# Kernel optimization log

Measured on AMD Instinct MI355X. Metric: run time of the kernel, lower is better.

Reference implementation:

```python
import jax, jax.numpy as jnp
import numpy as np

D_MODEL = 1024
C_OUT = 64
PRED_LEN = 96
D_STATE = 64
D_CONV = 4
EXPAND = 2
D_INNER = EXPAND * D_MODEL          # 2048
DT_RANK = D_MODEL // 16             # 64
IN_DIM = D_MODEL + C_OUT
BATCH = 512


def setup_inputs() -> dict:
    key = jax.random.key(0)
    ks = jax.random.split(key, 10)
    def w(k, shape, scale=0.02):
        return jax.random.normal(k, shape, dtype=jnp.float32) * scale
    return {
        "context": jax.random.normal(ks[0], (BATCH, D_MODEL), dtype=jnp.float32),
        "initial_values": jax.random.normal(ks[1], (BATCH, C_OUT), dtype=jnp.float32),
        "w_in": w(ks[2], (IN_DIM, 2 * D_INNER)),
        "b_in": jnp.zeros((2 * D_INNER,), jnp.float32),
        "conv_w": w(ks[3], (D_INNER, D_CONV)),
        "conv_b": jnp.zeros((D_INNER,), jnp.float32),
        "w_x": w(ks[4], (D_INNER, DT_RANK + 2 * D_STATE)),
        "w_dt": w(ks[5], (DT_RANK, D_INNER)),
        "b_dt": jnp.zeros((D_INNER,), jnp.float32),
        "A_log": jnp.log(jnp.broadcast_to(jnp.arange(1, D_STATE + 1, dtype=jnp.float32), (D_INNER, D_STATE))),
        "D_skip": jnp.ones((D_INNER,), jnp.float32),
        "w_out": w(ks[6], (D_INNER, D_MODEL)),
        "b_out": jnp.zeros((D_MODEL,), jnp.float32),
        "w_proj": w(ks[7], (D_MODEL, C_OUT)),
        "b_proj": jnp.zeros((C_OUT,), jnp.float32),
    }


def _mamba_len1(u, w_in, b_in, conv_w, conv_b, w_x, w_dt, b_dt, D_skip, w_out, b_out):
    """Standard Mamba block applied to a length-1 sequence (fresh state each call,
    matching the torch module, which calls mamba on [B,1,D] every step).
    With h0 = 0 and L = 1, the exp(dt*A) recurrence term vanishes, so A_log has no effect."""
    xz = u @ w_in + b_in                         # [B, 2*D_INNER]
    x, z = jnp.split(xz, 2, axis=-1)             # [B, D_INNER] each
    # causal depthwise conv over L=1: only the last kernel tap hits the current input
    x = x * conv_w[:, -1] + conv_b
    x = jax.nn.silu(x)
    xdbc = x @ w_x                               # [B, DT_RANK + 2*D_STATE]
    dt = jax.nn.softplus(xdbc[:, :DT_RANK] @ w_dt + b_dt)          # [B, D_INNER]
    Bm = xdbc[:, DT_RANK:DT_RANK + D_STATE]                         # [B, D_STATE]
    Cm = xdbc[:, DT_RANK + D_STATE:]                                # [B, D_STATE]
    # h = (dt*x)[:, :, None] * Bm[:, None, :]; y = sum_s h * Cm  ->  factored form
    y = (dt * x) * jnp.sum(Bm * Cm, axis=-1, keepdims=True)         # [B, D_INNER]
    y = y + D_skip * x
    y = y * jax.nn.silu(z)
    return y @ w_out + b_out                     # [B, D_MODEL]


def reference(context, initial_values, w_in, b_in, conv_w, conv_b, w_x, w_dt,
              b_dt, A_log, D_skip, w_out, b_out, w_proj, b_proj):
    del A_log  # no effect with fresh zero SSM state and seq_len=1 (see _mamba_len1)

    def step(prev_pred, _):
        u = jnp.concatenate([context, prev_pred], axis=-1)          # [B, IN_DIM]
        h = _mamba_len1(u, w_in, b_in, conv_w, conv_b, w_x, w_dt, b_dt,
                        D_skip, w_out, b_out)                        # [B, D_MODEL]
        pred = h @ w_proj + b_proj                                   # [B, C_OUT]
        return pred, pred

    _, preds = jax.lax.scan(step, initial_values, None, length=PRED_LEN)
    return jnp.transpose(preds, (1, 0, 2))       # [B, PRED_LEN, C_OUT]
```

## Files before the change

kernel.cpp:

```cpp
#include <hip/hip_runtime.h>
#include <math.h>


typedef __fp16 half2_t __attribute__((ext_vector_type(2)));
typedef unsigned int uint32;
union HU { uint32 u; half2_t h; };

__device__ __forceinline__ float sigf(float v){
  return __builtin_amdgcn_rcpf(1.f + __expf(-v));
}
__device__ __forceinline__ uint32 pk2(float a, float b){
  HU x; x.h = __builtin_amdgcn_cvt_pkrtz(a, b); return x.u;
}
__device__ __forceinline__ float dot2(uint32 a, uint32 b, float c){
  HU ua, ub; ua.u = a; ub.u = b;
  return __builtin_amdgcn_fdot2(ua.h, ub.h, c, false);
}


__global__ __launch_bounds__(256) void k_ctx(
    const float* __restrict__ ctxin, const float* __restrict__ w_in,
    const float* __restrict__ b_in, float* __restrict__ ctx_xz){
  int tid = threadIdx.x;
  int j = blockIdx.x*256 + tid;
  int b0 = blockIdx.y*16;
  const float* cp = ctxin + (size_t)b0*1024;
  float acc[16];
#pragma unroll
  for (int r=0;r<16;r++) acc[r]=0.f;
  for (int k=0;k<1024;k+=4){
    float w0 = w_in[(size_t)(k+0)*4096 + j];
    float w1 = w_in[(size_t)(k+1)*4096 + j];
    float w2 = w_in[(size_t)(k+2)*4096 + j];
    float w3 = w_in[(size_t)(k+3)*4096 + j];
#pragma unroll
    for (int r=0;r<16;r++){
      acc[r] += cp[r*1024+k]*w0 + cp[r*1024+k+1]*w1
              + cp[r*1024+k+2]*w2 + cp[r*1024+k+3]*w3;
    }
  }
  float bj = b_in[j];
#pragma unroll
  for (int r=0;r<16;r++) ctx_xz[(size_t)(b0+r)*4096 + j] = acc[r] + bj;
}

__global__ __launch_bounds__(256) void k_wop(
    const float* __restrict__ w_out, const float* __restrict__ w_proj,
    const float* __restrict__ b_out, const float* __restrict__ b_proj,
    float* __restrict__ W_op, float* __restrict__ b_op){
  int g = blockIdx.x, tid = threadIdx.x;
  if (g == 512){
    if (tid < 64){
      float s = b_proj[tid];
      for (int k=0;k<1024;k++) s += b_out[k]*w_proj[k*64+tid];
      b_op[tid] = s;
    }
    return;
  }
  int idx = g*256 + tid;
  int c = idx>>6, o = idx&63;
  float s = 0.f;
  const float* wr = w_out + (size_t)c*1024;
  for (int k=0;k<1024;k++) s += wr[k]*w_proj[k*64+o];
  W_op[idx] = s;
}

__global__ __launch_bounds__(256) void k_cvec(
    const float* __restrict__ b_op, const float* __restrict__ w_in2,
    float* __restrict__ cvec){
  int j = blockIdx.x*256 + threadIdx.x;
  float s = 0.f;
  for (int o=0;o<64;o++) s += b_op[o]*w_in2[(size_t)o*4096 + j];
  cvec[j] = s;
}

__global__ __launch_bounds__(256) void k_pack(
    const float* __restrict__ src, uint32* __restrict__ dst,
    int inner, int total){
  int idx = blockIdx.x*256 + threadIdx.x;
  if (idx >= total) return;
  int p = idx / inner, i = idx - p*inner;
  dst[idx] = pk2(src[(size_t)(2*p)*inner + i], src[(size_t)(2*p+1)*inner + i]);
}

__global__ __launch_bounds__(256) void k_pack_wx(
    const float* __restrict__ w_x, uint32* __restrict__ dst){
  int idx = blockIdx.x*256 + threadIdx.x;
  int q = idx & 3;
  int t = idx >> 2;
  int n = t % 192;
  int g = t / 192;
  int k2 = g*4 + q;
  dst[idx] = pk2(w_x[(size_t)(2*k2)*192 + n], w_x[(size_t)(2*k2+1)*192 + n]);
}

__global__ __launch_bounds__(256) void k_pack_wop(
    const float* __restrict__ W_op, uint32* __restrict__ dst){
  int idx = blockIdx.x*256 + threadIdx.x;
  int q = idx & 3;
  int t = idx >> 2;
  int o = t & 63;
  int g = t >> 6;
  int k2 = g*4 + q;
  dst[idx] = pk2(W_op[(size_t)(2*k2)*64 + o], W_op[(size_t)(2*k2+1)*64 + o]);
}

__global__ __launch_bounds__(256) void k_pack_wdt(
    const float* __restrict__ w_dt, uint32* __restrict__ dst){
  int idx = blockIdx.x*256 + threadIdx.x;
  int e = idx & 3;
  int t = idx >> 2;
  int c2 = t & 1023;
  int jp = t >> 10;
  int p = jp*2 + (e>>1);
  int c = c2*2 + (e&1);
  dst[idx] = pk2(w_dt[(size_t)(2*p)*2048 + c], w_dt[(size_t)(2*p+1)*2048 + c]);
}


__global__ __launch_bounds__(1024,4) void k_steps(
    const float* __restrict__ ctx_xz, const float* __restrict__ cvec,
    const uint32* __restrict__ h_in2p, const float* __restrict__ conv_w,
    const float* __restrict__ conv_b,  const uint32* __restrict__ wxp4,
    const uint32* __restrict__ wdtp4,  const float* __restrict__ b_dt,
    const float* __restrict__ D_skip,  const uint32* __restrict__ wopp4,
    const float* __restrict__ b_op,    const float* __restrict__ initial,
    float* __restrict__ dout)
{
  const int tid = threadIdx.x;
  const int r0  = blockIdx.x * 2;

  __shared__ uint2  predH2[32];
  __shared__ __align__(16) uint32 xbufH[2][1024];
  __shared__ float  zbuf[2][2048];
  __shared__ uint4  xdh2q[16];
  __shared__ float  bcL[2];
  __shared__ float  pxd[4][388];
  __shared__ float  ppd[16][130];
  __shared__ uint4  wxpin[6144];

  {
    const uint4* src = (const uint4*)wxp4;
#pragma unroll
    for (int i = tid; i < 6144; i += 1024){
      int ks = i / 1536;
      wxpin[i] = src[i + ks*10752];
    }
  }

  const int cb = tid*4;
  const bool isx = (cb < 2048);
  float4 cw4, cb4;
  if (isx){
    cw4 = make_float4(conv_w[(cb+0)*4+3], conv_w[(cb+1)*4+3],
                      conv_w[(cb+2)*4+3], conv_w[(cb+3)*4+3]);
    cb4 = *(const float4*)&conv_b[cb];
  }
  const float4 cv4   = *(const float4*)&cvec[cb];
  const float4 ctxr0 = *(const float4*)&ctx_xz[(size_t)(r0+0)*4096 + cb];
  const float4 ctxr1 = *(const float4*)&ctx_xz[(size_t)(r0+1)*4096 + cb];
  const int c2t = tid*2;
  const float2 bdt2 = *(const float2*)&b_dt[c2t];
  const float2 dsk2 = *(const float2*)&D_skip[c2t];
  const int n2  = tid % 192;
  const int ks2 = tid / 192;
  const int o4  = tid & 63;
  const int kb2 = (tid >> 6) * 64;
  const float bopv = b_op[(tid>>1) & 63];

  if (tid < 128){
    float v = initial[(size_t)(r0 + (tid&1))*64 + (tid>>1)];
    float vp = __shfl_down(v, 2, 64);
    if ((tid & 2) == 0)
      ((uint32*)predH2)[(tid>>2)*2 + (tid&1)] = pk2(v, vp);
  }
  __syncthreads();

  for (int t=0; t<96; t++){
    const float tf = (t > 0) ? 1.f : 0.f;
    float a0[4], a1[4];
#pragma unroll
    for (int i=0;i<4;i++){
      float c = (&cv4.x)[i];
      a0[i] = (&ctxr0.x)[i] + tf*c;
      a1[i] = (&ctxr1.x)[i] + tf*c;
    }
    {
      const uint32* wp = h_in2p + cb;
#pragma unroll 8
      for (int o2=0;o2<32;o2++){
        uint4 w  = *(const uint4*)&wp[(size_t)o2*4096];
        uint2 pd = *((const uint2*)predH2 + o2);
        a0[0]=dot2(w.x,pd.x,a0[0]); a0[1]=dot2(w.y,pd.x,a0[1]);
        a0[2]=dot2(w.z,pd.x,a0[2]); a0[3]=dot2(w.w,pd.x,a0[3]);
        a1[0]=dot2(w.x,pd.y,a1[0]); a1[1]=dot2(w.y,pd.y,a1[1]);
        a1[2]=dot2(w.z,pd.y,a1[2]); a1[3]=dot2(w.w,pd.y,a1[3]);
      }
    }
    if (isx){
      float x0[4], x1[4];
#pragma unroll
      for (int i=0;i<4;i++){
        float v0 = a0[i]*(&cw4.x)[i] + (&cb4.x)[i];
        float v1 = a1[i]*(&cw4.x)[i] + (&cb4.x)[i];
        x0[i] = v0*sigf(v0);
        x1[i] = v1*sigf(v1);
      }
      const int p = cb >> 1;
      *(uint2*)&xbufH[0][p] = make_uint2(pk2(x0[0], x0[1]), pk2(x0[2], x0[3]));
      *(uint2*)&xbufH[1][p] = make_uint2(pk2(x1[0], x1[1]), pk2(x1[2], x1[3]));
    } else {
      float4 z0, z1;
#pragma unroll
      for (int i=0;i<4;i++){
        (&z0.x)[i] = a0[i]*sigf(a0[i]);
        (&z1.x)[i] = a1[i]*sigf(a1[i]);
      }
      *(float4*)&zbuf[0][cb-2048] = z0;
      *(float4*)&zbuf[1][cb-2048] = z1;
    }
    __syncthreads();

    if (tid < 768){
      const uint4* wpin = &wxpin[ks2*1536 + n2];
      const uint4* wp4  = (const uint4*)wxp4 + (size_t)ks2*12288 + n2;
      const uint4* xb0  = (const uint4*)&xbufH[0][ks2*256];
      const uint4* xb1  = (const uint4*)&xbufH[1][ks2*256];
      float f0 = 0.f, f1 = 0.f;
#pragma unroll
      for (int j=0;j<8;j++){
        uint4 w  = wpin[j*192];
        uint4 x0 = xb0[j];
        uint4 x1 = xb1[j];
        f0 = dot2(w.x, x0.x, f0); f1 = dot2(w.x, x1.x, f1);
        f0 = dot2(w.y, x0.y, f0); f1 = dot2(w.y, x1.y, f1);
        f0 = dot2(w.z, x0.z, f0); f1 = dot2(w.z, x1.z, f1);
        f0 = dot2(w.w, x0.w, f0); f1 = dot2(w.w, x1.w, f1);
      }
#pragma unroll 8
      for (int j=8;j<64;j++){
        uint4 w  = wp4[(size_t)j*192];
        uint4 x0 = xb0[j];
        uint4 x1 = xb1[j];
        f0 = dot2(w.x, x0.x, f0); f1 = dot2(w.x, x1.x, f1);
        f0 = dot2(w.y, x0.y, f0); f1 = dot2(w.y, x1.y, f1);
        f0 = dot2(w.z, x0.z, f0); f1 = dot2(w.z, x1.z, f1);
        f0 = dot2(w.w, x0.w, f0); f1 = dot2(w.w, x1.w, f1);
      }
      *(float2*)&pxd[ks2][n2*2] = make_float2(f0, f1);
    }
    __syncthreads();

    if (tid < 128){
      int r = tid >> 6, nl = tid & 63;
      int ib = (64+nl)*2 + r, ic = (128+nl)*2 + r;
      float bv = pxd[0][ib] + pxd[1][ib] + pxd[2][ib] + pxd[3][ib];
      float cv = pxd[0][ic] + pxd[1][ic] + pxd[2][ic] + pxd[3][ic];
      float p = bv * cv;
#pragma unroll
      for (int sh=1; sh<64; sh<<=1) p += __shfl_xor(p, sh, 64);
      if (nl == 0) bcL[r] = p;
    } else if (tid < 160){
      int o2 = tid - 128;
      int i00 = (2*o2)*2, i10 = (2*o2+1)*2;
      float v00 = pxd[0][i00  ] + pxd[1][i00  ] + pxd[2][i00  ] + pxd[3][i00  ];
      float v01 = pxd[0][i00+1] + pxd[1][i00+1] + pxd[2][i00+1] + pxd[3][i00+1];
      float v10 = pxd[0][i10  ] + pxd[1][i10  ] + pxd[2][i10  ] + pxd[3][i10  ];
      float v11 = pxd[0][i10+1] + pxd[1][i10+1] + pxd[2][i10+1] + pxd[3][i10+1];
      ((uint32*)xdh2q)[o2*2+0] = pk2(v00, v10);
      ((uint32*)xdh2q)[o2*2+1] = pk2(v01, v11);
    }
    __syncthreads();

    float d00=0.f, d01=0.f, d10=0.f, d11=0.f;
    {
      const uint4* wd4 = (const uint4*)wdtp4 + tid;
#pragma unroll 8
      for (int jp=0;jp<16;jp++){
        uint4 w  = wd4[(size_t)jp*1024];
        uint4 xd = xdh2q[jp];
        d00 = dot2(w.x, xd.x, d00);
        d01 = dot2(w.y, xd.x, d01);
        d10 = dot2(w.x, xd.y, d10);
        d11 = dot2(w.y, xd.y, d11);
        d00 = dot2(w.z, xd.z, d00);
        d01 = dot2(w.w, xd.z, d01);
        d10 = dot2(w.z, xd.w, d10);
        d11 = dot2(w.w, xd.w, d11);
      }
    }
    {
      float bc0 = bcL[0], bc1 = bcL[1];
      HU xh0, xh1; xh0.u = xbufH[0][tid]; xh1.u = xbufH[1][tid];
      float2 zr0 = *(const float2*)&zbuf[0][c2t];
      float2 zr1 = *(const float2*)&zbuf[1][c2t];
      float v00 = d00 + bdt2.x, v01 = d01 + bdt2.y;
      float v10 = d10 + bdt2.x, v11 = d11 + bdt2.y;
      float s00 = (v00 > 15.f) ? v00 : __logf(1.f + __expf(v00));
      float s01 = (v01 > 15.f) ? v01 : __logf(1.f + __expf(v01));
      float s10 = (v10 > 15.f) ? v10 : __logf(1.f + __expf(v10));
      float s11 = (v11 > 15.f) ? v11 : __logf(1.f + __expf(v11));
      float y00 = (s00*bc0 + dsk2.x) * (float)xh0.h.x * zr0.x;
      float y01 = (s01*bc0 + dsk2.y) * (float)xh0.h.y * zr0.y;
      float y10 = (s10*bc1 + dsk2.x) * (float)xh1.h.x * zr1.x;
      float y11 = (s11*bc1 + dsk2.y) * (float)xh1.h.y * zr1.y;
      xbufH[0][tid] = pk2(y00, y01);
      xbufH[1][tid] = pk2(y10, y11);
    }
    __syncthreads();

    {
      const uint4* wo4 = (const uint4*)wopp4 + (size_t)(tid>>6)*1024 + o4;
      const uint4* yb0 = (const uint4*)&xbufH[0][kb2];
      const uint4* yb1 = (const uint4*)&xbufH[1][kb2];
      float p0 = 0.f, p1 = 0.f;
#pragma unroll 8
      for (int j=0;j<16;j++){
        uint4 w  = wo4[(size_t)j*64];
        uint4 y0 = yb0[j];
        uint4 y1 = yb1[j];
        p0 = dot2(w.x, y0.x, p0); p1 = dot2(w.x, y1.x, p1);
        p0 = dot2(w.y, y0.y, p0); p1 = dot2(w.y, y1.y, p1);
        p0 = dot2(w.z, y0.z, p0); p1 = dot2(w.z, y1.z, p1);
        p0 = dot2(w.w, y0.w, p0); p1 = dot2(w.w, y1.w, p1);
      }
      *(float2*)&ppd[tid>>6][o4*2] = make_float2(p0, p1);
    }
    __syncthreads();

    if (tid < 128){
      float v = 0.f;
#pragma unroll
      for (int ks=0; ks<16; ks++) v += ppd[ks][tid];
      int o = tid >> 1, r = tid & 1;
      dout[((size_t)(r0+r)*96 + t)*64 + o] = v + bopv;
      float vp = __shfl_down(v, 2, 64);
      if ((tid & 2) == 0)
        ((uint32*)predH2)[(tid>>2)*2 + (tid&1)] = pk2(v, vp);
    }
    __syncthreads();
  }
}


extern "C" void kernel_launch(void* const* d_in, const int* in_sizes, int n_in,
                              void* d_out, int out_size, void* d_ws, size_t ws_size,
                              hipStream_t stream)
{
  const float* context = (const float*)d_in[0];
  const float* initial = (const float*)d_in[1];
  const float* w_in    = (const float*)d_in[2];
  const float* b_in    = (const float*)d_in[3];
  const float* conv_w  = (const float*)d_in[4];
  const float* conv_b  = (const float*)d_in[5];
  const float* w_x     = (const float*)d_in[6];
  const float* w_dt    = (const float*)d_in[7];
  const float* b_dt    = (const float*)d_in[8];
  const float* D_skip  = (const float*)d_in[10];
  const float* w_out   = (const float*)d_in[11];
  const float* b_out   = (const float*)d_in[12];
  const float* w_proj  = (const float*)d_in[13];
  const float* b_proj  = (const float*)d_in[14];

  float* ws = (float*)d_ws;
  float*  ctx_xz = ws;
  float*  cvec   = ctx_xz + 2097152;
  float*  W_op   = cvec + 4096;
  float*  b_op   = W_op + 131072;
  uint32* h_in2p = (uint32*)(b_op + 128);
  uint32* wxp4   = h_in2p + 131072;
  uint32* wdtp4  = wxp4 + 196608;
  uint32* wopp4  = wdtp4 + 65536;
  float*  dout   = (float*)d_out;

  const float* w_in2 = w_in + (size_t)1024*4096;

  k_wop     <<<dim3(513),   256, 0, stream>>>(w_out, w_proj, b_out, b_proj, W_op, b_op);
  k_cvec    <<<dim3(16),    256, 0, stream>>>(b_op, w_in2, cvec);
  k_ctx     <<<dim3(16,32), 256, 0, stream>>>(context, w_in, b_in, ctx_xz);
  k_pack    <<<dim3(512),   256, 0, stream>>>(w_in2, h_in2p, 4096, 131072);
  k_pack_wx <<<dim3(768),   256, 0, stream>>>(w_x,  wxp4);
  k_pack_wdt<<<dim3(256),   256, 0, stream>>>(w_dt, wdtp4);
  k_pack_wop<<<dim3(256),   256, 0, stream>>>(W_op, wopp4);

  k_steps<<<dim3(256), 1024, 0, stream>>>(ctx_xz, cvec, h_in2p, conv_w, conv_b,
                                          wxp4, wdtp4, b_dt, D_skip, wopp4, b_op,
                                          initial, dout);
}
```

Before: 2.082 ms.

## Replace per-step block barriers with redundant per-wave reductions and private LDS buffers

Two of the `__syncthreads` calls per time step are removed. Every wavefront now redundantly computes the B·C dot product, the packed dt-rank vector and the next prediction vector into its own LDS slot (`xdh2qW`, `predH2W`), so no cross-wave hand-off is needed. An `s_waitcnt lgkmcnt(0)` fence orders the LDS accesses within each wave, and the output store becomes a float2 store from wave 0. This trades extra redundant LDS reads and ALU work across 16 waves for fewer block-wide barriers in the 96-step serial loop.

```diff
diff --git a/kernel.cpp b/kernel.cpp
--- a/kernel.cpp
+++ b/kernel.cpp
@@ -15,6 +15,9 @@
 __device__ __forceinline__ float dot2(uint32 a, uint32 b, float c){
   HU ua, ub; ua.u = a; ub.u = b;
   return __builtin_amdgcn_fdot2(ua.h, ub.h, c, false);
+}
+__device__ __forceinline__ void ldsfence(){
+  asm volatile("s_waitcnt lgkmcnt(0)" ::: "memory");
 }
 
 
@@ -127,21 +130,21 @@
     const float* __restrict__ b_op,    const float* __restrict__ initial,
     float* __restrict__ dout)
 {
-  const int tid = threadIdx.x;
-  const int r0  = blockIdx.x * 2;
-
-  __shared__ uint2  predH2[32];
+  const int tid  = threadIdx.x;
+  const int wid  = tid >> 6;
+  const int lane = tid & 63;
+  const int r0   = blockIdx.x * 2;
+
   __shared__ __align__(16) uint32 xbufH[2][1024];
   __shared__ float  zbuf[2][2048];
-  __shared__ uint4  xdh2q[16];
-  __shared__ float  bcL[2];
   __shared__ float  pxd[4][388];
   __shared__ float  ppd[16][130];
   __shared__ uint4  wxpin[6144];
+  __shared__ uint32 predH2W[16][64];
+  __shared__ uint4  xdh2qW[16][16];
 
   {
     const uint4* src = (const uint4*)wxp4;
-#pragma unroll
     for (int i = tid; i < 6144; i += 1024){
       int ks = i / 1536;
       wxpin[i] = src[i + ks*10752];
@@ -166,13 +169,13 @@
   const int ks2 = tid / 192;
   const int o4  = tid & 63;
   const int kb2 = (tid >> 6) * 64;
-  const float bopv = b_op[(tid>>1) & 63];
-
-  if (tid < 128){
-    float v = initial[(size_t)(r0 + (tid&1))*64 + (tid>>1)];
-    float vp = __shfl_down(v, 2, 64);
-    if ((tid & 2) == 0)
-      ((uint32*)predH2)[(tid>>2)*2 + (tid&1)] = pk2(v, vp);
+  const float2 bop2 = *(const float2*)&b_op[lane & ~1];
+
+  {
+    int q = lane>>1, b = lane&1;
+    float va = initial[(size_t)(r0+b)*64 + 2*q];
+    float vc = initial[(size_t)(r0+b)*64 + 2*q + 1];
+    predH2W[wid][lane] = pk2(va, vc);
   }
   __syncthreads();
 
@@ -187,10 +190,11 @@
     }
     {
       const uint32* wp = h_in2p + cb;
+      const uint2* pdW = (const uint2*)&predH2W[wid][0];
 #pragma unroll 8
       for (int o2=0;o2<32;o2++){
         uint4 w  = *(const uint4*)&wp[(size_t)o2*4096];
-        uint2 pd = *((const uint2*)predH2 + o2);
+        uint2 pd = pdW[o2];
         a0[0]=dot2(w.x,pd.x,a0[0]); a0[1]=dot2(w.y,pd.x,a0[1]);
         a0[2]=dot2(w.z,pd.x,a0[2]); a0[3]=dot2(w.w,pd.x,a0[3]);
         a1[0]=dot2(w.x,pd.y,a1[0]); a1[1]=dot2(w.y,pd.y,a1[1]);
@@ -251,26 +255,33 @@
     }
     __syncthreads();
 
-    if (tid < 128){
-      int r = tid >> 6, nl = tid & 63;
-      int ib = (64+nl)*2 + r, ic = (128+nl)*2 + r;
-      float bv = pxd[0][ib] + pxd[1][ib] + pxd[2][ib] + pxd[3][ib];
-      float cv = pxd[0][ic] + pxd[1][ic] + pxd[2][ic] + pxd[3][ic];
-      float p = bv * cv;
-#pragma unroll
-      for (int sh=1; sh<64; sh<<=1) p += __shfl_xor(p, sh, 64);
-      if (nl == 0) bcL[r] = p;
-    } else if (tid < 160){
-      int o2 = tid - 128;
-      int i00 = (2*o2)*2, i10 = (2*o2+1)*2;
-      float v00 = pxd[0][i00  ] + pxd[1][i00  ] + pxd[2][i00  ] + pxd[3][i00  ];
-      float v01 = pxd[0][i00+1] + pxd[1][i00+1] + pxd[2][i00+1] + pxd[3][i00+1];
-      float v10 = pxd[0][i10  ] + pxd[1][i10  ] + pxd[2][i10  ] + pxd[3][i10  ];
-      float v11 = pxd[0][i10+1] + pxd[1][i10+1] + pxd[2][i10+1] + pxd[3][i10+1];
-      ((uint32*)xdh2q)[o2*2+0] = pk2(v00, v10);
-      ((uint32*)xdh2q)[o2*2+1] = pk2(v01, v11);
-    }
-    __syncthreads();
+    float bc0, bc1;
+    {
+      int ib0 = (64+lane)*2, ic0 = (128+lane)*2;
+      float bv0 = pxd[0][ib0]+pxd[1][ib0]+pxd[2][ib0]+pxd[3][ib0];
+      float cv0 = pxd[0][ic0]+pxd[1][ic0]+pxd[2][ic0]+pxd[3][ic0];
+      float p0 = bv0*cv0;
+      int ib1 = ib0+1, ic1 = ic0+1;
+      float bv1 = pxd[0][ib1]+pxd[1][ib1]+pxd[2][ib1]+pxd[3][ib1];
+      float cv1 = pxd[0][ic1]+pxd[1][ic1]+pxd[2][ic1]+pxd[3][ic1];
+      float p1 = bv1*cv1;
+#pragma unroll
+      for (int sh=1; sh<64; sh<<=1){
+        p0 += __shfl_xor(p0, sh, 64);
+        p1 += __shfl_xor(p1, sh, 64);
+      }
+      bc0 = p0; bc1 = p1;
+      if (lane < 32){
+        int o2 = lane;
+        int i00 = (2*o2)*2, i10 = (2*o2+1)*2;
+        float v00 = pxd[0][i00  ]+pxd[1][i00  ]+pxd[2][i00  ]+pxd[3][i00  ];
+        float v01 = pxd[0][i00+1]+pxd[1][i00+1]+pxd[2][i00+1]+pxd[3][i00+1];
+        float v10 = pxd[0][i10  ]+pxd[1][i10  ]+pxd[2][i10  ]+pxd[3][i10  ];
+        float v11 = pxd[0][i10+1]+pxd[1][i10+1]+pxd[2][i10+1]+pxd[3][i10+1];
+        ((uint2*)&xdh2qW[wid][0])[o2] = make_uint2(pk2(v00, v10), pk2(v01, v11));
+      }
+      ldsfence();
+    }
 
     float d00=0.f, d01=0.f, d10=0.f, d11=0.f;
     {
@@ -278,7 +289,7 @@
 #pragma unroll 8
       for (int jp=0;jp<16;jp++){
         uint4 w  = wd4[(size_t)jp*1024];
-        uint4 xd = xdh2q[jp];
+        uint4 xd = xdh2qW[wid][jp];
         d00 = dot2(w.x, xd.x, d00);
         d01 = dot2(w.y, xd.x, d01);
         d10 = dot2(w.x, xd.y, d10);
@@ -290,7 +301,6 @@
       }
     }
     {
-      float bc0 = bcL[0], bc1 = bcL[1];
       HU xh0, xh1; xh0.u = xbufH[0][tid]; xh1.u = xbufH[1][tid];
       float2 zr0 = *(const float2*)&zbuf[0][c2t];
       float2 zr1 = *(const float2*)&zbuf[1][c2t];
@@ -328,17 +338,22 @@
     }
     __syncthreads();
 
-    if (tid < 128){
-      float v = 0.f;
-#pragma unroll
-      for (int ks=0; ks<16; ks++) v += ppd[ks][tid];
-      int o = tid >> 1, r = tid & 1;
-      dout[((size_t)(r0+r)*96 + t)*64 + o] = v + bopv;
-      float vp = __shfl_down(v, 2, 64);
-      if ((tid & 2) == 0)
-        ((uint32*)predH2)[(tid>>2)*2 + (tid&1)] = pk2(v, vp);
-    }
-    __syncthreads();
+    {
+      int q = lane>>1, b = lane&1;
+      int a = 4*q + b;
+      float va = 0.f, vc = 0.f;
+#pragma unroll
+      for (int ks=0; ks<16; ks++){
+        va += ppd[ks][a];
+        vc += ppd[ks][a+2];
+      }
+      if (wid == 0){
+        float* dp = &dout[((size_t)(r0+b)*96 + t)*64 + 2*q];
+        *(float2*)dp = make_float2(va + bop2.x, vc + bop2.y);
+      }
+      predH2W[wid][lane] = pk2(va, vc);
+      ldsfence();
+    }
   }
 }
 
```

Result: slower. 2.142 ms (+2.9%).
